# Kernel optimization log

Measured on AMD Instinct MI355X. Metric: run time of the kernel, lower is better.

## Reference

```python
import jax, jax.numpy as jnp
import numpy as np


def setup_inputs() -> dict:
    key = jax.random.key(0)
    k1, k2 = jax.random.split(key)
    preds = jax.random.normal(k1, (16, 4096, 3), dtype=jnp.float32)
    gts = jax.random.normal(k2, (16, 4096, 3), dtype=jnp.float32)
    return {"preds": preds, "gts": gts}


def _pairwise_sqdist(x, y):
    # x: [B, N1, D], y: [B, N2, D] -> P: [B, N1, N2]
    rx = jnp.sum(x * x, axis=-1)  # [B, N1]
    ry = jnp.sum(y * y, axis=-1)  # [B, N2]
    zz = jnp.einsum("bnd,bmd->bnm", x, y)  # [B, N1, N2]
    return rx[:, :, None] + ry[:, None, :] - 2.0 * zz


def reference(preds, gts):
    # Symmetric Hausdorff distance (squared-dist version) per batch element.
    P = _pairwise_sqdist(preds, gts)  # [B, N1, N2]
    # min over preds (axis 1) for each gt point, then max over gt points
    loss1 = jnp.max(jnp.min(P, axis=1), axis=1)  # [B]
    # min over gts (axis 2) for each pred point, then max over pred points
    loss2 = jnp.max(jnp.min(P, axis=2), axis=1)  # [B]
    return (loss1 + loss2) * 0.5
```

## Files before the change

### kernel.cpp

```cpp
#include <hip/hip_runtime.h>
#include <math.h>


#define NPTS 4096
#define NB 16
#define TPB 256
#define WAVES 4
#define GPW 64
#define GPB (WAVES * GPW)
#define NGB (NPTS / GPB)
#define SPLIT 8
#define OPP (NPTS / SPLIT)
#define TILES (OPP / 32)

#define WSMIN_N (2 * NB * NPTS)

typedef _Float16 h8 __attribute__((ext_vector_type(8)));
typedef float f16v __attribute__((ext_vector_type(16)));

template <int CTRL>
__device__ __forceinline__ float min_dpp(float v) {
    int s = __builtin_amdgcn_update_dpp(0, __float_as_int(v), CTRL, 0xF, 0xF, true);
    return fminf(v, __int_as_float(s));
}

__global__ __launch_bounds__(TPB) void haus_scan_kernel(
        const float* __restrict__ preds, const float* __restrict__ gts,
        unsigned int* __restrict__ wsmin) {
    const int gt  = blockIdx.x & (NGB - 1);
    const int sp  = blockIdx.x >> 4;
    const int b   = blockIdx.y;
    const int t   = threadIdx.x;
    const int lane = t & 63, w = t >> 6;
    const int l31 = lane & 31, half = lane >> 5;

    const float* gbp = gts   + (size_t)b * NPTS * 3;
    const float* pbp = preds + (size_t)b * NPTS * 3;

    __shared__ h8 srec[2 * OPP];
    __shared__ float scol[8 * OPP];

#pragma unroll
    for (int i = 0; i < OPP / TPB; ++i) {
        int p = i * TPB + t;
        const float* s = pbp + (size_t)(sp * OPP + p) * 3;
        float x = s[0], y = s[1], z = s[2];
        float hp = fmaf(x, x, fmaf(y, y, z * z));
        _Float16 xh = (_Float16)x, yh = (_Float16)y, zh = (_Float16)z;
        _Float16 xl = (_Float16)(x - (float)xh);
        _Float16 yl = (_Float16)(y - (float)yh);
        _Float16 zl = (_Float16)(z - (float)zh);
        _Float16 hph = (_Float16)hp, hpl = (_Float16)(hp - (float)hph);
        h8 lo, hi;
        lo[0] = xh; lo[1] = yh; lo[2] = zh;
        lo[3] = xl; lo[4] = yl; lo[5] = zl;
        lo[6] = xh; lo[7] = yh;
        hi[0] = zh;
        hi[1] = hph; hi[2] = hpl;
        hi[3] = (_Float16)1; hi[4] = (_Float16)1;
        hi[5] = (_Float16)0; hi[6] = (_Float16)0; hi[7] = (_Float16)0;
        srec[p] = lo;
        srec[OPP + p] = hi;
    }

    h8 afrag[2];
#pragma unroll
    for (int a = 0; a < 2; ++a) {
        int m = gt * GPB + w * GPW + a * 32 + l31;
        float gx = gbp[m * 3 + 0], gy = gbp[m * 3 + 1], gz = gbp[m * 3 + 2];
        float hg = fmaf(gx, gx, fmaf(gy, gy, gz * gz));
        _Float16 gxh = (_Float16)gx, gyh = (_Float16)gy, gzh = (_Float16)gz;
        _Float16 gxl = (_Float16)(gx - (float)gxh);
        _Float16 gyl = (_Float16)(gy - (float)gyh);
        _Float16 gzl = (_Float16)(gz - (float)gzh);
        _Float16 hgh = (_Float16)hg, hgl = (_Float16)(hg - (float)hgh);
        const _Float16 n2 = (_Float16)(-2.0f);
        h8 f;
        if (half == 0) {
            f[0] = n2 * gxh; f[1] = n2 * gyh; f[2] = n2 * gzh;
            f[3] = n2 * gxh; f[4] = n2 * gyh; f[5] = n2 * gzh;
            f[6] = n2 * gxl; f[7] = n2 * gyl;
        } else {
            f[0] = n2 * gzl;
            f[1] = (_Float16)1; f[2] = (_Float16)1;
            f[3] = hgh; f[4] = hgl;
            f[5] = (_Float16)0; f[6] = (_Float16)0; f[7] = (_Float16)0;
        }
        afrag[a] = f;
    }

    f16v zc = {};
    float best0[16], best1[16];
#pragma unroll
    for (int r = 0; r < 16; ++r) { best0[r] = INFINITY; best1[r] = INFINITY; }

    __syncthreads();

    const h8* sptr = srec + half * OPP + l31;
    float* scw = scol + (w * 2 + half) * OPP + l31;
#pragma unroll 4
    for (int tt = 0; tt < TILES; ++tt) {
        h8 bfrag = sptr[tt * 32];
        f16v D0 = __builtin_amdgcn_mfma_f32_32x32x16_f16(afrag[0], bfrag, zc, 0, 0, 0);
        f16v D1 = __builtin_amdgcn_mfma_f32_32x32x16_f16(afrag[1], bfrag, zc, 0, 0, 0);
#pragma unroll
        for (int r = 0; r < 16; ++r) best0[r] = fminf(best0[r], D0[r]);
#pragma unroll
        for (int r = 0; r < 16; ++r) best1[r] = fminf(best1[r], D1[r]);
        float c8[8];
#pragma unroll
        for (int r = 0; r < 8; ++r)
            c8[r] = fminf(fminf(D0[2 * r], D0[2 * r + 1]),
                          fminf(D1[2 * r], D1[2 * r + 1]));
        float c0 = fminf(fminf(c8[0], c8[1]), fminf(c8[2], c8[3]));
        float c1 = fminf(fminf(c8[4], c8[5]), fminf(c8[6], c8[7]));
        scw[tt * 32] = fminf(c0, c1);
    }

#pragma unroll
    for (int r = 0; r < 16; ++r) {
        float a0 = best0[r], a1 = best1[r];
        a0 = min_dpp<0x121>(a0); a1 = min_dpp<0x121>(a1);
        a0 = min_dpp<0x122>(a0); a1 = min_dpp<0x122>(a1);
        a0 = min_dpp<0x124>(a0); a1 = min_dpp<0x124>(a1);
        a0 = min_dpp<0x128>(a0); a1 = min_dpp<0x128>(a1);
        float s0 = __int_as_float(__builtin_amdgcn_ds_swizzle(__float_as_int(a0), 0x401F));
        float s1 = __int_as_float(__builtin_amdgcn_ds_swizzle(__float_as_int(a1), 0x401F));
        best0[r] = fminf(a0, s0);
        best1[r] = fminf(a1, s1);
    }
    unsigned int* wsrow = wsmin + ((size_t)0 * NB + b) * NPTS + gt * GPB + w * GPW;
    if (l31 == 0) {
#pragma unroll
        for (int r = 0; r < 16; ++r) {
            int row = (r & 3) + 8 * (r >> 2) + 4 * half;
            float d0 = fmaxf(best0[r], 0.0f);
            float d1 = fmaxf(best1[r], 0.0f);
            atomicMin(wsrow + row, __float_as_uint(d0));
            atomicMin(wsrow + 32 + row, __float_as_uint(d1));
        }
    }

    __syncthreads();
    unsigned int* wscol = wsmin + ((size_t)1 * NB + b) * NPTS + sp * OPP;
#pragma unroll
    for (int i = 0; i < OPP / TPB; ++i) {
        int p = i * TPB + t;
        float m = scol[p];
#pragma unroll
        for (int k = 1; k < 8; ++k) m = fminf(m, scol[k * OPP + p]);
        atomicMin(wscol + p, __float_as_uint(fmaxf(m, 0.0f)));
    }
}

__global__ __launch_bounds__(TPB) void haus_final_kernel(
        const unsigned int* __restrict__ wsmin, float* __restrict__ out) {
    const int b = blockIdx.x;
    const int t = threadIdx.x;
    const float4* w0 = (const float4*)(wsmin + ((size_t)0 * NB + b) * NPTS);
    const float4* w1 = (const float4*)(wsmin + ((size_t)1 * NB + b) * NPTS);
    float m1 = -INFINITY, m2 = -INFINITY;
#pragma unroll
    for (int r = 0; r < NPTS / 4 / TPB; ++r) {
        float4 a = w0[r * TPB + t];
        float4 c = w1[r * TPB + t];
        m1 = fmaxf(fmaxf(fmaxf(a.x, a.y), fmaxf(a.z, a.w)), m1);
        m2 = fmaxf(fmaxf(fmaxf(c.x, c.y), fmaxf(c.z, c.w)), m2);
    }
#pragma unroll
    for (int off = 32; off > 0; off >>= 1) {
        m1 = fmaxf(m1, __shfl_down(m1, off, 64));
        m2 = fmaxf(m2, __shfl_down(m2, off, 64));
    }
    __shared__ float s1[4], s2[4];
    if ((t & 63) == 0) { s1[t >> 6] = m1; s2[t >> 6] = m2; }
    __syncthreads();
    if (t == 0) {
        float a = fmaxf(fmaxf(s1[0], s1[1]), fmaxf(s1[2], s1[3]));
        float c = fmaxf(fmaxf(s2[0], s2[1]), fmaxf(s2[2], s2[3]));
        out[b] = 0.5f * (a + c);
    }
}

extern "C" void kernel_launch(void* const* d_in, const int* in_sizes, int n_in,
                              void* d_out, int out_size, void* d_ws, size_t ws_size,
                              hipStream_t stream) {
    const float* preds = (const float*)d_in[0];
    const float* gts   = (const float*)d_in[1];
    float* out = (float*)d_out;
    unsigned int* wsmin = (unsigned int*)d_ws;

    hipMemsetAsync(wsmin, 0xFF, (size_t)WSMIN_N * sizeof(unsigned int), stream);

    haus_scan_kernel<<<dim3(NGB * SPLIT, NB, 1), dim3(TPB), 0, stream>>>(
        preds, gts, wsmin);

    haus_final_kernel<<<dim3(NB), dim3(TPB), 0, stream>>>(wsmin, out);
}
```

Measured before the change: 89.11 us.

## Precompute fp16 split-precision point records in a separate prep kernel

Adds a prep kernel that converts both point clouds into fp16 hi/lo MFMA operand records once and stores them in the workspace. The scan kernel then reads A and B fragments straight from global memory instead of rebuilding them per block in shared memory, which removes the shared staging and its barrier. Launch bounds now request 8 blocks per unit to raise occupancy. The cost is an extra kernel launch, extra global traffic for the records, and B fragments now come through global/L2 rather than LDS.

Result: slower. 247.2 us (+177.4%).

```diff
diff --git a/kernel.cpp b/kernel.cpp
--- a/kernel.cpp
+++ b/kernel.cpp
@@ -14,6 +14,8 @@
 #define TILES (OPP / 32)
 
 #define WSMIN_N (2 * NB * NPTS)
+#define RECA_OFF (WSMIN_N * 4)
+#define RECB_OFF (RECA_OFF + NB * 2 * NPTS * 16)
 
 typedef _Float16 h8 __attribute__((ext_vector_type(8)));
 typedef float f16v __attribute__((ext_vector_type(16)));
@@ -24,26 +26,35 @@
     return fminf(v, __int_as_float(s));
 }
 
-__global__ __launch_bounds__(TPB) void haus_scan_kernel(
+__global__ __launch_bounds__(TPB) void haus_prep_kernel(
         const float* __restrict__ preds, const float* __restrict__ gts,
-        unsigned int* __restrict__ wsmin) {
-    const int gt  = blockIdx.x & (NGB - 1);
-    const int sp  = blockIdx.x >> 4;
-    const int b   = blockIdx.y;
-    const int t   = threadIdx.x;
-    const int lane = t & 63, w = t >> 6;
-    const int l31 = lane & 31, half = lane >> 5;
-
-    const float* gbp = gts   + (size_t)b * NPTS * 3;
-    const float* pbp = preds + (size_t)b * NPTS * 3;
-
-    __shared__ h8 srec[2 * OPP];
-    __shared__ float scol[8 * OPP];
-
-#pragma unroll
-    for (int i = 0; i < OPP / TPB; ++i) {
-        int p = i * TPB + t;
-        const float* s = pbp + (size_t)(sp * OPP + p) * 3;
+        h8* __restrict__ recA, h8* __restrict__ recB) {
+    int idx = blockIdx.x * TPB + threadIdx.x;
+    int b = idx >> 12, i = idx & (NPTS - 1);
+    const _Float16 n2 = (_Float16)(-2.0f);
+
+    {
+        const float* s = gts + (size_t)b * NPTS * 3 + (size_t)i * 3;
+        float x = s[0], y = s[1], z = s[2];
+        float hg = fmaf(x, x, fmaf(y, y, z * z));
+        _Float16 xh = (_Float16)x, yh = (_Float16)y, zh = (_Float16)z;
+        _Float16 xl = (_Float16)(x - (float)xh);
+        _Float16 yl = (_Float16)(y - (float)yh);
+        _Float16 zl = (_Float16)(z - (float)zh);
+        _Float16 hgh = (_Float16)hg, hgl = (_Float16)(hg - (float)hgh);
+        h8 lo, hi;
+        lo[0] = n2 * xh; lo[1] = n2 * yh; lo[2] = n2 * zh;
+        lo[3] = n2 * xh; lo[4] = n2 * yh; lo[5] = n2 * zh;
+        lo[6] = n2 * xl; lo[7] = n2 * yl;
+        hi[0] = n2 * zl;
+        hi[1] = (_Float16)1; hi[2] = (_Float16)1;
+        hi[3] = hgh; hi[4] = hgl;
+        hi[5] = (_Float16)0; hi[6] = (_Float16)0; hi[7] = (_Float16)0;
+        recA[((size_t)b * 2 + 0) * NPTS + i] = lo;
+        recA[((size_t)b * 2 + 1) * NPTS + i] = hi;
+    }
+    {
+        const float* s = preds + (size_t)b * NPTS * 3 + (size_t)i * 3;
         float x = s[0], y = s[1], z = s[2];
         float hp = fmaf(x, x, fmaf(y, y, z * z));
         _Float16 xh = (_Float16)x, yh = (_Float16)y, zh = (_Float16)z;
@@ -59,50 +70,40 @@
         hi[1] = hph; hi[2] = hpl;
         hi[3] = (_Float16)1; hi[4] = (_Float16)1;
         hi[5] = (_Float16)0; hi[6] = (_Float16)0; hi[7] = (_Float16)0;
-        srec[p] = lo;
-        srec[OPP + p] = hi;
-    }
-
-    h8 afrag[2];
-#pragma unroll
-    for (int a = 0; a < 2; ++a) {
-        int m = gt * GPB + w * GPW + a * 32 + l31;
-        float gx = gbp[m * 3 + 0], gy = gbp[m * 3 + 1], gz = gbp[m * 3 + 2];
-        float hg = fmaf(gx, gx, fmaf(gy, gy, gz * gz));
-        _Float16 gxh = (_Float16)gx, gyh = (_Float16)gy, gzh = (_Float16)gz;
-        _Float16 gxl = (_Float16)(gx - (float)gxh);
-        _Float16 gyl = (_Float16)(gy - (float)gyh);
-        _Float16 gzl = (_Float16)(gz - (float)gzh);
-        _Float16 hgh = (_Float16)hg, hgl = (_Float16)(hg - (float)hgh);
-        const _Float16 n2 = (_Float16)(-2.0f);
-        h8 f;
-        if (half == 0) {
-            f[0] = n2 * gxh; f[1] = n2 * gyh; f[2] = n2 * gzh;
-            f[3] = n2 * gxh; f[4] = n2 * gyh; f[5] = n2 * gzh;
-            f[6] = n2 * gxl; f[7] = n2 * gyl;
-        } else {
-            f[0] = n2 * gzl;
-            f[1] = (_Float16)1; f[2] = (_Float16)1;
-            f[3] = hgh; f[4] = hgl;
-            f[5] = (_Float16)0; f[6] = (_Float16)0; f[7] = (_Float16)0;
-        }
-        afrag[a] = f;
-    }
+        recB[((size_t)b * 2 + 0) * NPTS + i] = lo;
+        recB[((size_t)b * 2 + 1) * NPTS + i] = hi;
+    }
+}
+
+__global__ __launch_bounds__(TPB, 8) void haus_scan_kernel(
+        const h8* __restrict__ recA, const h8* __restrict__ recB,
+        unsigned int* __restrict__ wsmin) {
+    const int gt  = blockIdx.x & (NGB - 1);
+    const int sp  = blockIdx.x >> 4;
+    const int b   = blockIdx.y;
+    const int t   = threadIdx.x;
+    const int lane = t & 63, w = t >> 6;
+    const int l31 = lane & 31, half = lane >> 5;
+
+    __shared__ float scol[8 * OPP];
+
+    const h8* rA = recA + ((size_t)b * 2 + half) * NPTS + gt * GPB + w * GPW + l31;
+    h8 afrag0 = rA[0];
+    h8 afrag1 = rA[32];
+
+    const h8* rB = recB + ((size_t)b * 2 + half) * NPTS + sp * OPP + l31;
+    float* scw = scol + (w * 2 + half) * OPP + l31;
 
     f16v zc = {};
     float best0[16], best1[16];
 #pragma unroll
     for (int r = 0; r < 16; ++r) { best0[r] = INFINITY; best1[r] = INFINITY; }
 
-    __syncthreads();
-
-    const h8* sptr = srec + half * OPP + l31;
-    float* scw = scol + (w * 2 + half) * OPP + l31;
 #pragma unroll 4
     for (int tt = 0; tt < TILES; ++tt) {
-        h8 bfrag = sptr[tt * 32];
-        f16v D0 = __builtin_amdgcn_mfma_f32_32x32x16_f16(afrag[0], bfrag, zc, 0, 0, 0);
-        f16v D1 = __builtin_amdgcn_mfma_f32_32x32x16_f16(afrag[1], bfrag, zc, 0, 0, 0);
+        h8 bfrag = rB[tt * 32];
+        f16v D0 = __builtin_amdgcn_mfma_f32_32x32x16_f16(afrag0, bfrag, zc, 0, 0, 0);
+        f16v D1 = __builtin_amdgcn_mfma_f32_32x32x16_f16(afrag1, bfrag, zc, 0, 0, 0);
 #pragma unroll
         for (int r = 0; r < 16; ++r) best0[r] = fminf(best0[r], D0[r]);
 #pragma unroll
@@ -189,11 +190,16 @@
     const float* gts   = (const float*)d_in[1];
     float* out = (float*)d_out;
     unsigned int* wsmin = (unsigned int*)d_ws;
+    h8* recA = (h8*)((char*)d_ws + RECA_OFF);
+    h8* recB = (h8*)((char*)d_ws + RECB_OFF);
 
     hipMemsetAsync(wsmin, 0xFF, (size_t)WSMIN_N * sizeof(unsigned int), stream);
 
+    haus_prep_kernel<<<dim3(NB * NPTS / TPB), dim3(TPB), 0, stream>>>(
+        preds, gts, recA, recB);
+
     haus_scan_kernel<<<dim3(NGB * SPLIT, NB, 1), dim3(TPB), 0, stream>>>(
-        preds, gts, wsmin);
+        recA, recB, wsmin);
 
     haus_final_kernel<<<dim3(NB), dim3(TPB), 0, stream>>>(wsmin, out);
 }
```
